# Kernel optimization log

Hardware: AMD Instinct MI355X
Metric: run time of the kernel (lower is better)

The kernel has to match this reference:

```python
import jax, jax.numpy as jnp
import numpy as np

N, E, R, D = 100000, 300000, 2, 128


def setup_inputs() -> dict:
    key = jax.random.key(0)
    k0, k1, k2, k3, k4 = jax.random.split(key, 5)
    x = jax.random.normal(k0, (N, D), dtype=jnp.float32)
    attn_w = jax.random.normal(k1, (R, 2 * D), dtype=jnp.float32) / np.sqrt(2 * D).astype(np.float32)
    loop_weight = jax.random.normal(k2, (D, D), dtype=jnp.float32) / np.sqrt(D).astype(np.float32)
    h_bias = jnp.zeros((D,), dtype=jnp.float32)
    src = jax.random.randint(k3, (R, E), 0, N, dtype=jnp.int32)
    dst = jax.random.randint(k4, (R, E), 0, N, dtype=jnp.int32)
    return {"x": x, "attn_w": attn_w, "loop_weight": loop_weight, "h_bias": h_bias,
            "src": src, "dst": dst}


def _rel_attention(x, a, src_r, dst_r):
    # Per-edge score: attn_fc(cat(src feat, dst feat)) with Linear(2D -> 1, no bias).
    d = x.shape[1]
    xs = x[src_r]                     # [E, D] gathered source features (the messages m)
    e = xs @ a[:d] + x[dst_r] @ a[d:]  # [E] edge logits (note: no leaky_relu in message_fc path)
    # Segment (per-destination mailbox) softmax, numerically stable.
    m = jax.ops.segment_max(e, dst_r, num_segments=N)
    p = jnp.exp(e - m[dst_r])
    denom = jax.ops.segment_sum(p, dst_r, num_segments=N)
    alpha = p / jnp.maximum(denom[dst_r], jnp.float32(1e-30))  # [E]
    # Weighted scatter-sum of messages back to destination nodes.
    return jax.ops.segment_sum(alpha[:, None] * xs, dst_r, num_segments=N)  # [N, D]


def reference(x, attn_w, loop_weight, h_bias, src, dst):
    # multi_update_all(..., 'sum'): sum the per-relation attention aggregations.
    agg = _rel_attention(x, attn_w[0], src[0], dst[0])
    for r in range(1, R):
        agg = agg + _rel_attention(x, attn_w[r], src[r], dst[r])
    # self loop + bias (activation=None, dropout=0)
    h = agg + x @ loop_weight + h_bias
    return h
```

## Files before the change

### kernel.cpp

```cpp
#include <hip/hip_runtime.h>

#define N_NODES 100000
#define N_EDGES 300000
#define DIM     128
#define NBINS   (2 * N_NODES)
#define CNT_STRIDE 16
#define SLOT_CAP 16
#define ROW_TILES (N_NODES / 16)
#define GDIM (DIM + 4)
#define BATCH 4

#define WCONV_BLOCKS 8
#define ZERO_BLOCKS ((NBINS * CNT_STRIDE / 4 + 255) / 256)
#define BIN2_BLOCKS ((N_EDGES / 2 + 255) / 256)
#define SC_BLOCKS   1024
#define SC_WAVES    (SC_BLOCKS * 4)

typedef __attribute__((ext_vector_type(8))) short bfrag;
typedef __attribute__((ext_vector_type(4))) float f32x4;
typedef __attribute__((ext_vector_type(2))) unsigned int   u32x2;

__device__ __forceinline__ unsigned short f2bf(float f) {
  unsigned int u = __float_as_uint(f);
  u += 0x7FFFu + ((u >> 16) & 1u);
  return (unsigned short)(u >> 16);
}
__device__ __forceinline__ float bflo(unsigned int u) { return __uint_as_float(u << 16); }
__device__ __forceinline__ float bfhi(unsigned int u) { return __uint_as_float(u & 0xffff0000u); }

__global__ __launch_bounds__(256) void k0_kernel(
    int* __restrict__ counts, unsigned short* __restrict__ Wt,
    const float* __restrict__ W) {
  if (blockIdx.x < WCONV_BLOCKS) {
    for (int e = blockIdx.x * 256 + threadIdx.x; e < DIM * DIM; e += WCONV_BLOCKS * 256) {
      int k = e >> 7, c = e & 127;
      Wt[c * DIM + k] = f2bf(W[e]);
    }
    return;
  }
  int i = (blockIdx.x - WCONV_BLOCKS) * 256 + threadIdx.x;
  if (i < NBINS * CNT_STRIDE / 4) ((int4*)counts)[i] = make_int4(0, 0, 0, 0);
}

__global__ __launch_bounds__(256) void k1_kernel(
    const float* __restrict__ x, const float* __restrict__ attn_w,
    const int* __restrict__ src, const int* __restrict__ dst,
    float* __restrict__ pexp, int* __restrict__ counts, int* __restrict__ slots,
    unsigned short* __restrict__ x_bf) {
  int tid = threadIdx.x;
  if (blockIdx.x < BIN2_BLOCKS) {
    int t = blockIdx.x * 256 + tid;
    if (t < N_EDGES / 2) {
      int ea = t, eb = t + N_EDGES / 2;
      int da0 = __builtin_nontemporal_load(&dst[ea]);
      int db0 = __builtin_nontemporal_load(&dst[eb]);
      int da1 = __builtin_nontemporal_load(&dst[ea + N_EDGES]);
      int db1 = __builtin_nontemporal_load(&dst[eb + N_EDGES]);
      int sa0 = __builtin_nontemporal_load(&src[ea]);
      int sb0 = __builtin_nontemporal_load(&src[eb]);
      int sa1 = __builtin_nontemporal_load(&src[ea + N_EDGES]);
      int sb1 = __builtin_nontemporal_load(&src[eb + N_EDGES]);
      int pa0 = atomicAdd(&counts[(size_t)(da0 * 2 + 0) * CNT_STRIDE], 1);
      int pb0 = atomicAdd(&counts[(size_t)(db0 * 2 + 0) * CNT_STRIDE], 1);
      int pa1 = atomicAdd(&counts[(size_t)(da1 * 2 + 1) * CNT_STRIDE], 1);
      int pb1 = atomicAdd(&counts[(size_t)(db1 * 2 + 1) * CNT_STRIDE], 1);
      if (pa0 < SLOT_CAP)
        __builtin_nontemporal_store(sa0, &slots[(size_t)(da0 * 2 + 0) * SLOT_CAP + pa0]);
      if (pb0 < SLOT_CAP)
        __builtin_nontemporal_store(sb0, &slots[(size_t)(db0 * 2 + 0) * SLOT_CAP + pb0]);
      if (pa1 < SLOT_CAP)
        __builtin_nontemporal_store(sa1, &slots[(size_t)(da1 * 2 + 1) * SLOT_CAP + pa1]);
      if (pb1 < SLOT_CAP)
        __builtin_nontemporal_store(sb1, &slots[(size_t)(db1 * 2 + 1) * SLOT_CAP + pb1]);
    }
    return;
  }
  int wave = (((blockIdx.x - BIN2_BLOCKS) * 256) + tid) >> 6;
  int l    = tid & 63;
  int h    = l >> 5;
  int l32  = l & 31;
  f32x4 a0 = ((const f32x4*)(attn_w +   0))[l32];
  f32x4 a1 = ((const f32x4*)(attn_w + 256))[l32];
  for (int base = wave * 2; base < N_NODES; base += SC_WAVES * 2) {
    int n = base + h;
    if (n >= N_NODES) continue;
    f32x4 v = __builtin_nontemporal_load(((const f32x4*)(x + (size_t)n * DIM)) + l32);
    unsigned int lo = ((unsigned int)f2bf(v.y) << 16) | f2bf(v.x);
    unsigned int hi = ((unsigned int)f2bf(v.w) << 16) | f2bf(v.z);
    ((u32x2*)(x_bf + (size_t)n * DIM))[l32] = (u32x2){lo, hi};
    float p0 = v.x*a0.x + v.y*a0.y + v.z*a0.z + v.w*a0.w;
    float p1 = v.x*a1.x + v.y*a1.y + v.z*a1.z + v.w*a1.w;
    #pragma unroll
    for (int off = 16; off > 0; off >>= 1) {
      p0 += __shfl_xor(p0, off, 64);
      p1 += __shfl_xor(p1, off, 64);
    }
    if (l32 == 0) {
      pexp[n]           = __expf(p0);
      pexp[N_NODES + n] = __expf(p1);
    }
  }
}

__global__ __launch_bounds__(256) void k2_kernel(
    const int* __restrict__ slots, const int* __restrict__ counts,
    const float* __restrict__ pexp, const unsigned short* __restrict__ x_bf,
    const unsigned short* __restrict__ Wt, const float* __restrict__ bias,
    float* __restrict__ out) {
  __shared__ float gtile[16][GDIM];
  int tid = threadIdx.x;
  int r0  = blockIdx.x * 16;
  int w   = tid >> 6;
  int wl  = tid & 63;
  int rrel  = wl >> 5;
  int l     = wl & 31;
  int nbase = r0 + w * 4;
  int craw[4], sraw[4];
  #pragma unroll
  for (int nn = 0; nn < 4; nn++)
    craw[nn] = __builtin_nontemporal_load(
        &counts[(size_t)((nbase + nn) * 2 + rrel) * CNT_STRIDE]);
  #pragma unroll
  for (int nn = 0; nn < 4; nn++)
    sraw[nn] = __builtin_nontemporal_load(
        &slots[(size_t)((nbase + nn) * 2 + rrel) * SLOT_CAP + (l & 15)]);
  {
    int n = wl & 15, q = wl >> 4;
    const unsigned short* xrow = x_bf + (size_t)(r0 + n) * DIM;
    f32x4 acc[2];
    #pragma unroll
    for (int c = 0; c < 2; c++) {
      float bv = bias[(2 * w + c) * 16 + n];
      acc[c] = (f32x4){bv, bv, bv, bv};
    }
    #pragma unroll
    for (int kc = 0; kc < 4; kc++) {
      int k0 = kc * 32 + q * 8;
      bfrag a = *((const bfrag*)(xrow + k0));
      #pragma unroll
      for (int c = 0; c < 2; c++) {
        bfrag b = *((const bfrag*)(Wt + (size_t)((2 * w + c) * 16 + n) * DIM + k0));
        acc[c] = __builtin_amdgcn_mfma_f32_16x16x32_bf16(a, b, acc[c], 0, 0, 0);
      }
    }
    #pragma unroll
    for (int c = 0; c < 2; c++)
      #pragma unroll
      for (int rr = 0; rr < 4; rr++)
        gtile[q * 4 + rr][(2 * w + c) * 16 + n] = acc[c][rr];
  }
  int cnt[4]; int sj[4];
  #pragma unroll
  for (int nn = 0; nn < 4; nn++) {
    cnt[nn] = (craw[nn] > SLOT_CAP) ? SLOT_CAP : craw[nn];
    sj[nn]  = (l < cnt[nn]) ? sraw[nn] : 0;
  }
  u32x2 g[4][BATCH];
  #pragma unroll
  for (int u = 0; u < BATCH; u++) {
    #pragma unroll
    for (int nn = 0; nn < 4; nn++) {
      int s = __shfl(sj[nn], u, 32);
      g[nn][u] = ((const u32x2*)(x_bf + (size_t)s * DIM))[l];
    }
  }
  float pl[4];
  #pragma unroll
  for (int nn = 0; nn < 4; nn++)
    pl[nn] = pexp[rrel * N_NODES + sj[nn]];
  float pj[4]; float dinv[4];
  #pragma unroll
  for (int nn = 0; nn < 4; nn++) {
    pj[nn] = (l < cnt[nn]) ? pl[nn] : 0.f;
    float d = pj[nn];
    #pragma unroll
    for (int off = 16; off > 0; off >>= 1) d += __shfl_xor(d, off, 64);
    dinv[nn] = (cnt[nn] > 0) ? 1.f / d : 0.f;
  }
  f32x4 accr[4];
  #pragma unroll
  for (int nn = 0; nn < 4; nn++) accr[nn] = (f32x4){0.f, 0.f, 0.f, 0.f};
  #pragma unroll
  for (int nn = 0; nn < 4; nn++) {
    #pragma unroll
    for (int u = 0; u < BATCH; u++) {
      float qv = __shfl(pj[nn], u, 32);
      u32x2 gv = g[nn][u];
      accr[nn].x += qv * bflo(gv.x);
      accr[nn].y += qv * bfhi(gv.x);
      accr[nn].z += qv * bflo(gv.y);
      accr[nn].w += qv * bfhi(gv.y);
    }
  }
  #pragma unroll
  for (int nn = 0; nn < 4; nn++) {
    int cn = cnt[nn];
    int j = BATCH;
    for (; j + 4 <= cn; j += 4) {
      int   s0 = __shfl(sj[nn], j + 0, 32); float q0 = __shfl(pj[nn], j + 0, 32);
      int   s1 = __shfl(sj[nn], j + 1, 32); float q1 = __shfl(pj[nn], j + 1, 32);
      int   s2 = __shfl(sj[nn], j + 2, 32); float q2 = __shfl(pj[nn], j + 2, 32);
      int   s3 = __shfl(sj[nn], j + 3, 32); float q3 = __shfl(pj[nn], j + 3, 32);
      u32x2 g0 = ((const u32x2*)(x_bf + (size_t)s0 * DIM))[l];
      u32x2 g1 = ((const u32x2*)(x_bf + (size_t)s1 * DIM))[l];
      u32x2 g2 = ((const u32x2*)(x_bf + (size_t)s2 * DIM))[l];
      u32x2 g3 = ((const u32x2*)(x_bf + (size_t)s3 * DIM))[l];
      accr[nn].x += q0*bflo(g0.x) + q1*bflo(g1.x) + q2*bflo(g2.x) + q3*bflo(g3.x);
      accr[nn].y += q0*bfhi(g0.x) + q1*bfhi(g1.x) + q2*bfhi(g2.x) + q3*bfhi(g3.x);
      accr[nn].z += q0*bflo(g0.y) + q1*bflo(g1.y) + q2*bflo(g2.y) + q3*bflo(g3.y);
      accr[nn].w += q0*bfhi(g0.y) + q1*bfhi(g1.y) + q2*bfhi(g2.y) + q3*bfhi(g3.y);
    }
    for (; j < cn; j++) {
      int   s0 = __shfl(sj[nn], j, 32); float q0 = __shfl(pj[nn], j, 32);
      u32x2 g0 = ((const u32x2*)(x_bf + (size_t)s0 * DIM))[l];
      accr[nn].x += q0*bflo(g0.x); accr[nn].y += q0*bfhi(g0.x);
      accr[nn].z += q0*bflo(g0.y); accr[nn].w += q0*bfhi(g0.y);
    }
  }
  __syncthreads();
  #pragma unroll
  for (int nn = 0; nn < 4; nn++) {
    f32x4 agg;
    agg.x = accr[nn].x * dinv[nn];
    agg.y = accr[nn].y * dinv[nn];
    agg.z = accr[nn].z * dinv[nn];
    agg.w = accr[nn].w * dinv[nn];
    agg.x += __shfl_xor(agg.x, 32, 64);
    agg.y += __shfl_xor(agg.y, 32, 64);
    agg.z += __shfl_xor(agg.z, 32, 64);
    agg.w += __shfl_xor(agg.w, 32, 64);
    if (wl < 32) {
      const float* gr = &gtile[w * 4 + nn][4 * wl];
      f32x4 o;
      o.x = gr[0] + agg.x; o.y = gr[1] + agg.y;
      o.z = gr[2] + agg.z; o.w = gr[3] + agg.w;
      __builtin_nontemporal_store(o, (f32x4*)(out + (size_t)(r0 + w * 4 + nn) * DIM) + wl);
    }
  }
}

extern "C" void kernel_launch(void* const* d_in, const int* in_sizes, int n_in,
                              void* d_out, int out_size, void* d_ws, size_t ws_size,
                              hipStream_t stream) {
  const float* x      = (const float*)d_in[0];
  const float* attn_w = (const float*)d_in[1];
  const float* loop_w = (const float*)d_in[2];
  const float* h_bias = (const float*)d_in[3];
  const int*   src    = (const int*)d_in[4];
  const int*   dst    = (const int*)d_in[5];
  float*       out    = (float*)d_out;

  float*          pexp   = (float*)d_ws;
  int*            counts = (int*)(pexp + NBINS);
  int*            slots  = counts + (size_t)NBINS * CNT_STRIDE;
  unsigned short* Wt     = (unsigned short*)(slots + (size_t)NBINS * SLOT_CAP);
  unsigned short* x_bf   = Wt + DIM * DIM;

  k0_kernel<<<WCONV_BLOCKS + ZERO_BLOCKS, 256, 0, stream>>>(counts, Wt, loop_w);
  k1_kernel<<<BIN2_BLOCKS + SC_BLOCKS, 256, 0, stream>>>(
      x, attn_w, src, dst, pexp, counts, slots, x_bf);
  k2_kernel<<<ROW_TILES, 256, 0, stream>>>(
      slots, counts, pexp, x_bf, Wt, h_bias, out);
}
```

Measured before the change: 220.0 us.

## Pack per-bin count and first slots into one 64-byte line with overflow

Each destination bin now stores its atomic counter and first 15 source indices together in one 16-int line, with a separate overflow array for up to 16 more edges. The consumer reads count and slots in one load instead of two separate strided arrays. The goal is fewer cache lines touched in binning and gather, and the capacity rises from 16 to 31, which improves correctness for high-degree nodes. In exchange, the rare overflow path adds serial loads and one fewer inline slot.

```diff
diff --git a/kernel.cpp b/kernel.cpp
--- a/kernel.cpp
+++ b/kernel.cpp
@@ -4,14 +4,15 @@
 #define N_EDGES 300000
 #define DIM     128
 #define NBINS   (2 * N_NODES)
-#define CNT_STRIDE 16
-#define SLOT_CAP 16
+#define BINW    16
+#define SLOT_INLINE 15
+#define CAP_TOTAL   31
 #define ROW_TILES (N_NODES / 16)
 #define GDIM (DIM + 4)
 #define BATCH 4
 
 #define WCONV_BLOCKS 8
-#define ZERO_BLOCKS ((NBINS * CNT_STRIDE / 4 + 255) / 256)
+#define ZERO_BLOCKS ((NBINS * BINW / 4 + 255) / 256)
 #define BIN2_BLOCKS ((N_EDGES / 2 + 255) / 256)
 #define SC_BLOCKS   1024
 #define SC_WAVES    (SC_BLOCKS * 4)
@@ -29,7 +30,7 @@
 __device__ __forceinline__ float bfhi(unsigned int u) { return __uint_as_float(u & 0xffff0000u); }
 
 __global__ __launch_bounds__(256) void k0_kernel(
-    int* __restrict__ counts, unsigned short* __restrict__ Wt,
+    int* __restrict__ bins, unsigned short* __restrict__ Wt,
     const float* __restrict__ W) {
   if (blockIdx.x < WCONV_BLOCKS) {
     for (int e = blockIdx.x * 256 + threadIdx.x; e < DIM * DIM; e += WCONV_BLOCKS * 256) {
@@ -39,13 +40,24 @@
     return;
   }
   int i = (blockIdx.x - WCONV_BLOCKS) * 256 + threadIdx.x;
-  if (i < NBINS * CNT_STRIDE / 4) ((int4*)counts)[i] = make_int4(0, 0, 0, 0);
+  if (i < NBINS * BINW / 4) ((int4*)bins)[i] = make_int4(0, 0, 0, 0);
+}
+
+__device__ __forceinline__ void bin_one(int d, int r, int s,
+                                        int* __restrict__ bins,
+                                        int* __restrict__ ovf) {
+  size_t base = (size_t)(d * 2 + r) * BINW;
+  int pos = atomicAdd(&bins[base], 1);
+  if (pos < SLOT_INLINE)
+    __builtin_nontemporal_store(s, &bins[base + 1 + pos]);
+  else if (pos < CAP_TOTAL)
+    __builtin_nontemporal_store(s, &ovf[base + (pos - SLOT_INLINE)]);
 }
 
 __global__ __launch_bounds__(256) void k1_kernel(
     const float* __restrict__ x, const float* __restrict__ attn_w,
     const int* __restrict__ src, const int* __restrict__ dst,
-    float* __restrict__ pexp, int* __restrict__ counts, int* __restrict__ slots,
+    float* __restrict__ pexp, int* __restrict__ bins, int* __restrict__ ovf,
     unsigned short* __restrict__ x_bf) {
   int tid = threadIdx.x;
   if (blockIdx.x < BIN2_BLOCKS) {
@@ -60,18 +72,10 @@
       int sb0 = __builtin_nontemporal_load(&src[eb]);
       int sa1 = __builtin_nontemporal_load(&src[ea + N_EDGES]);
       int sb1 = __builtin_nontemporal_load(&src[eb + N_EDGES]);
-      int pa0 = atomicAdd(&counts[(size_t)(da0 * 2 + 0) * CNT_STRIDE], 1);
-      int pb0 = atomicAdd(&counts[(size_t)(db0 * 2 + 0) * CNT_STRIDE], 1);
-      int pa1 = atomicAdd(&counts[(size_t)(da1 * 2 + 1) * CNT_STRIDE], 1);
-      int pb1 = atomicAdd(&counts[(size_t)(db1 * 2 + 1) * CNT_STRIDE], 1);
-      if (pa0 < SLOT_CAP)
-        __builtin_nontemporal_store(sa0, &slots[(size_t)(da0 * 2 + 0) * SLOT_CAP + pa0]);
-      if (pb0 < SLOT_CAP)
-        __builtin_nontemporal_store(sb0, &slots[(size_t)(db0 * 2 + 0) * SLOT_CAP + pb0]);
-      if (pa1 < SLOT_CAP)
-        __builtin_nontemporal_store(sa1, &slots[(size_t)(da1 * 2 + 1) * SLOT_CAP + pa1]);
-      if (pb1 < SLOT_CAP)
-        __builtin_nontemporal_store(sb1, &slots[(size_t)(db1 * 2 + 1) * SLOT_CAP + pb1]);
+      bin_one(da0, 0, sa0, bins, ovf);
+      bin_one(db0, 0, sb0, bins, ovf);
+      bin_one(da1, 1, sa1, bins, ovf);
+      bin_one(db1, 1, sb1, bins, ovf);
     }
     return;
   }
@@ -103,7 +107,7 @@
 }
 
 __global__ __launch_bounds__(256) void k2_kernel(
-    const int* __restrict__ slots, const int* __restrict__ counts,
+    const int* __restrict__ bins, const int* __restrict__ ovf,
     const float* __restrict__ pexp, const unsigned short* __restrict__ x_bf,
     const unsigned short* __restrict__ Wt, const float* __restrict__ bias,
     float* __restrict__ out) {
@@ -115,15 +119,11 @@
   int rrel  = wl >> 5;
   int l     = wl & 31;
   int nbase = r0 + w * 4;
-  int craw[4], sraw[4];
+  int braw[4];
   #pragma unroll
   for (int nn = 0; nn < 4; nn++)
-    craw[nn] = __builtin_nontemporal_load(
-        &counts[(size_t)((nbase + nn) * 2 + rrel) * CNT_STRIDE]);
-  #pragma unroll
-  for (int nn = 0; nn < 4; nn++)
-    sraw[nn] = __builtin_nontemporal_load(
-        &slots[(size_t)((nbase + nn) * 2 + rrel) * SLOT_CAP + (l & 15)]);
+    braw[nn] = __builtin_nontemporal_load(
+        &bins[(size_t)((nbase + nn) * 2 + rrel) * BINW + (l & 15)]);
   {
     int n = wl & 15, q = wl >> 4;
     const unsigned short* xrow = x_bf + (size_t)(r0 + n) * DIM;
@@ -149,18 +149,21 @@
       for (int rr = 0; rr < 4; rr++)
         gtile[q * 4 + rr][(2 * w + c) * 16 + n] = acc[c][rr];
   }
-  int cnt[4]; int sj[4];
-  #pragma unroll
-  for (int nn = 0; nn < 4; nn++) {
-    cnt[nn] = (craw[nn] > SLOT_CAP) ? SLOT_CAP : craw[nn];
-    sj[nn]  = (l < cnt[nn]) ? sraw[nn] : 0;
+  int srank = l - 1;
+  int craw[4], cext[4], cntA[4], sj[4];
+  #pragma unroll
+  for (int nn = 0; nn < 4; nn++) {
+    craw[nn] = __shfl(braw[nn], 0, 32);
+    cext[nn] = (craw[nn] > CAP_TOTAL) ? CAP_TOTAL : craw[nn];
+    cntA[nn] = (cext[nn] > SLOT_INLINE) ? SLOT_INLINE : cext[nn];
+    sj[nn]   = (srank >= 0 && srank < cntA[nn]) ? braw[nn] : 0;
   }
   u32x2 g[4][BATCH];
   #pragma unroll
   for (int u = 0; u < BATCH; u++) {
     #pragma unroll
     for (int nn = 0; nn < 4; nn++) {
-      int s = __shfl(sj[nn], u, 32);
+      int s = __shfl(sj[nn], u + 1, 32);
       g[nn][u] = ((const u32x2*)(x_bf + (size_t)s * DIM))[l];
     }
   }
@@ -171,11 +174,16 @@
   float pj[4]; float dinv[4];
   #pragma unroll
   for (int nn = 0; nn < 4; nn++) {
-    pj[nn] = (l < cnt[nn]) ? pl[nn] : 0.f;
+    pj[nn] = (srank >= 0 && srank < cntA[nn]) ? pl[nn] : 0.f;
     float d = pj[nn];
     #pragma unroll
     for (int off = 16; off > 0; off >>= 1) d += __shfl_xor(d, off, 64);
-    dinv[nn] = (cnt[nn] > 0) ? 1.f / d : 0.f;
+    if (craw[nn] > SLOT_INLINE) {
+      size_t obase = (size_t)((nbase + nn) * 2 + rrel) * BINW;
+      for (int j = SLOT_INLINE; j < cext[nn]; j++)
+        d += pexp[rrel * N_NODES + ovf[obase + (j - SLOT_INLINE)]];
+    }
+    dinv[nn] = (craw[nn] > 0) ? 1.f / d : 0.f;
   }
   f32x4 accr[4];
   #pragma unroll
@@ -184,7 +192,7 @@
   for (int nn = 0; nn < 4; nn++) {
     #pragma unroll
     for (int u = 0; u < BATCH; u++) {
-      float qv = __shfl(pj[nn], u, 32);
+      float qv = __shfl(pj[nn], u + 1, 32);
       u32x2 gv = g[nn][u];
       accr[nn].x += qv * bflo(gv.x);
       accr[nn].y += qv * bfhi(gv.x);
@@ -194,13 +202,13 @@
   }
   #pragma unroll
   for (int nn = 0; nn < 4; nn++) {
-    int cn = cnt[nn];
+    int cn = cntA[nn];
     int j = BATCH;
     for (; j + 4 <= cn; j += 4) {
-      int   s0 = __shfl(sj[nn], j + 0, 32); float q0 = __shfl(pj[nn], j + 0, 32);
-      int   s1 = __shfl(sj[nn], j + 1, 32); float q1 = __shfl(pj[nn], j + 1, 32);
-      int   s2 = __shfl(sj[nn], j + 2, 32); float q2 = __shfl(pj[nn], j + 2, 32);
-      int   s3 = __shfl(sj[nn], j + 3, 32); float q3 = __shfl(pj[nn], j + 3, 32);
+      int   s0 = __shfl(sj[nn], j + 1, 32); float q0 = __shfl(pj[nn], j + 1, 32);
+      int   s1 = __shfl(sj[nn], j + 2, 32); float q1 = __shfl(pj[nn], j + 2, 32);
+      int   s2 = __shfl(sj[nn], j + 3, 32); float q2 = __shfl(pj[nn], j + 3, 32);
+      int   s3 = __shfl(sj[nn], j + 4, 32); float q3 = __shfl(pj[nn], j + 4, 32);
       u32x2 g0 = ((const u32x2*)(x_bf + (size_t)s0 * DIM))[l];
       u32x2 g1 = ((const u32x2*)(x_bf + (size_t)s1 * DIM))[l];
       u32x2 g2 = ((const u32x2*)(x_bf + (size_t)s2 * DIM))[l];
@@ -211,10 +219,20 @@
       accr[nn].w += q0*bfhi(g0.y) + q1*bfhi(g1.y) + q2*bfhi(g2.y) + q3*bfhi(g3.y);
     }
     for (; j < cn; j++) {
-      int   s0 = __shfl(sj[nn], j, 32); float q0 = __shfl(pj[nn], j, 32);
+      int   s0 = __shfl(sj[nn], j + 1, 32); float q0 = __shfl(pj[nn], j + 1, 32);
       u32x2 g0 = ((const u32x2*)(x_bf + (size_t)s0 * DIM))[l];
       accr[nn].x += q0*bflo(g0.x); accr[nn].y += q0*bfhi(g0.x);
       accr[nn].z += q0*bflo(g0.y); accr[nn].w += q0*bfhi(g0.y);
+    }
+    if (craw[nn] > SLOT_INLINE) {
+      size_t obase = (size_t)((nbase + nn) * 2 + rrel) * BINW;
+      for (int j = SLOT_INLINE; j < cext[nn]; j++) {
+        int   sv = ovf[obase + (j - SLOT_INLINE)];
+        float qv = pexp[rrel * N_NODES + sv];
+        u32x2 g0 = ((const u32x2*)(x_bf + (size_t)sv * DIM))[l];
+        accr[nn].x += qv*bflo(g0.x); accr[nn].y += qv*bfhi(g0.x);
+        accr[nn].z += qv*bflo(g0.y); accr[nn].w += qv*bfhi(g0.y);
+      }
     }
   }
   __syncthreads();
@@ -250,15 +268,15 @@
   const int*   dst    = (const int*)d_in[5];
   float*       out    = (float*)d_out;
 
-  float*          pexp   = (float*)d_ws;
-  int*            counts = (int*)(pexp + NBINS);
-  int*            slots  = counts + (size_t)NBINS * CNT_STRIDE;
-  unsigned short* Wt     = (unsigned short*)(slots + (size_t)NBINS * SLOT_CAP);
-  unsigned short* x_bf   = Wt + DIM * DIM;
-
-  k0_kernel<<<WCONV_BLOCKS + ZERO_BLOCKS, 256, 0, stream>>>(counts, Wt, loop_w);
+  float*          pexp = (float*)d_ws;
+  int*            bins = (int*)(pexp + NBINS);
+  int*            ovf  = bins + (size_t)NBINS * BINW;
+  unsigned short* Wt   = (unsigned short*)(ovf + (size_t)NBINS * BINW);
+  unsigned short* x_bf = Wt + DIM * DIM;
+
+  k0_kernel<<<WCONV_BLOCKS + ZERO_BLOCKS, 256, 0, stream>>>(bins, Wt, loop_w);
   k1_kernel<<<BIN2_BLOCKS + SC_BLOCKS, 256, 0, stream>>>(
-      x, attn_w, src, dst, pexp, counts, slots, x_bf);
+      x, attn_w, src, dst, pexp, bins, ovf, x_bf);
   k2_kernel<<<ROW_TILES, 256, 0, stream>>>(
-      slots, counts, pexp, x_bf, Wt, h_bias, out);
-}
+      bins, ovf, pexp, x_bf, Wt, h_bias, out);
+}
```

New measurement: 227.5 us. +3.4%, slower.
